# Optimization experiments

Hardware: AMD Instinct MI355X
Metric: run time of the kernel (lower is better)

## Reference

```python
import jax, jax.numpy as jnp
import numpy as np

B, T, C = 2, 2048, 1024
H = 16
D = C // H  # 64
SCALE = 1.0 / np.sqrt(D)


def setup_inputs() -> dict:
    key = jax.random.key(0)
    k1, k2, k3 = jax.random.split(key, 3)
    x = jax.random.normal(k1, (B, T, C), dtype=jnp.float32)
    Wqkv = jax.random.normal(k2, (C, 3 * C), dtype=jnp.float32) * 0.02
    bqkv = jnp.zeros((3 * C,), dtype=jnp.float32)
    Wo = jax.random.normal(k3, (C, C), dtype=jnp.float32) * 0.02
    bo = jnp.zeros((C,), dtype=jnp.float32)
    return {"x": x, "Wqkv": Wqkv, "bqkv": bqkv, "Wo": Wo, "bo": bo}


def reference(x, Wqkv, bqkv, Wo, bo):
    Bsz, Tlen, Cdim = x.shape
    qkv = x @ Wqkv + bqkv                       # [B,T,3C]
    qkv = qkv.reshape(Bsz, Tlen, 3, H, D)
    qkv = jnp.transpose(qkv, (2, 0, 3, 1, 4))   # [3,B,H,T,D]
    q, k, v = qkv[0], qkv[1], qkv[2]
    att = jnp.einsum("bhqd,bhkd->bhqk", q, k) * SCALE
    # NOTE: faithful to source: mask keeps positions where k >= q
    i = jnp.arange(Tlen)
    mask = i[None, :] >= i[:, None]             # [T,T], entry [q,k]: k >= q
    att = jnp.where(mask[None, None], att, -jnp.inf)
    att = jax.nn.softmax(att, axis=-1)
    # dropout p=0.0 (inference) -> identity
    y = jnp.einsum("bhqk,bhkd->bhqd", att, v)   # [B,H,T,D]
    y = jnp.transpose(y, (0, 2, 1, 3)).reshape(Bsz, Tlen, Cdim)
    y = y @ Wo + bo
    return y
```

## Files before the change

### kernel.cpp

```cpp
#include <hip/hip_runtime.h>
#include <hip/hip_bf16.h>
#include <cstdint>
#include <cstddef>

typedef __bf16 bf16_t;
typedef __bf16 bf16x8 __attribute__((ext_vector_type(8)));
typedef __bf16 bf16x4 __attribute__((ext_vector_type(4)));
typedef short short4v __attribute__((ext_vector_type(4)));
typedef float f32x4 __attribute__((ext_vector_type(4)));

#define NB 2
#define NT 2048
#define NC 1024
#define NH 16
#define ND 64
#define NM (NB * NT)
#define N3 (3 * NC)
#define QSCALE_LOG2E 0.18033688011112042f

#define GLOAD_LDS16(gptr, lptr)                                                          \
  __builtin_amdgcn_global_load_lds((const __attribute__((address_space(1))) void*)(gptr), \
                                   (__attribute__((address_space(3))) void*)(lptr), 16, 0, 0)

__global__ __launch_bounds__(256) void prep_k(const float* __restrict__ x,
                                              const float* __restrict__ Wqkv,
                                              const float* __restrict__ Wo,
                                              bf16_t* __restrict__ xbf,
                                              bf16_t* __restrict__ wqkvT,
                                              bf16_t* __restrict__ woT) {
  __shared__ float tile[32][33];
  const int bx = blockIdx.x;
  if (bx < 4096) {
    const int i = (bx * 256 + threadIdx.x) * 4;
    const float4 v = *(const float4*)(x + i);
    bf16x4 o;
    o[0] = (bf16_t)v.x; o[1] = (bf16_t)v.y; o[2] = (bf16_t)v.z; o[3] = (bf16_t)v.w;
    *(bf16x4*)(xbf + i) = o;
    return;
  }
  const int t = bx - 4096;
  const int cxi = t & 127;
  const int tr = (t >> 7) * 32;
  const float* in;
  bf16_t* out;
  int Ccols, tc;
  if (cxi < 96) { in = Wqkv; out = wqkvT; Ccols = 3072; tc = cxi * 32; }
  else          { in = Wo;   out = woT;   Ccols = 1024; tc = (cxi - 96) * 32; }
  const int lx = threadIdx.x & 31;
  const int ly = threadIdx.x >> 5;
#pragma unroll
  for (int i = 0; i < 32; i += 8)
    tile[ly + i][lx] = in[(size_t)(tr + ly + i) * Ccols + tc + lx];
  __syncthreads();
#pragma unroll
  for (int i = 0; i < 32; i += 8)
    out[(size_t)(tc + ly + i) * 1024 + tr + lx] = (bf16_t)tile[lx][ly + i];
}

template <int K>
__device__ __forceinline__ void gemm_mainloop(const bf16_t* __restrict__ A,
                                              const bf16_t* __restrict__ Bt,
                                              int m0, int n0, f32x4 acc[4][4],
                                              bf16_t* lds) {
  bf16_t* As = lds;
  bf16_t* Bs = lds + 4096;
  const int tid = threadIdx.x;
  const int lane = tid & 63;
  const int w = tid >> 6;
  const int wm = (w & 1) * 64;
  const int wn = (w >> 1) * 64;
  const int quad = lane >> 4;
  const int l16 = lane & 15;

  for (int k0 = 0; k0 < K; k0 += 32) {
#pragma unroll
    for (int i = 0; i < 2; ++i) {
      const int gb = w * 128 + i * 64;
      const int g = gb + lane;
      GLOAD_LDS16(A + (size_t)(m0 + (g >> 2)) * K + k0 + (g & 3) * 8, As + gb * 8);
      GLOAD_LDS16(Bt + (size_t)(n0 + (g >> 2)) * K + k0 + (g & 3) * 8, Bs + gb * 8);
    }
    __syncthreads();
    bf16x8 af[4], bfr[4];
#pragma unroll
    for (int i = 0; i < 4; ++i)
      af[i] = *(const bf16x8*)(As + (wm + i * 16 + l16) * 32 + quad * 8);
#pragma unroll
    for (int j = 0; j < 4; ++j)
      bfr[j] = *(const bf16x8*)(Bs + (wn + j * 16 + l16) * 32 + quad * 8);
#pragma unroll
    for (int i = 0; i < 4; ++i)
#pragma unroll
      for (int j = 0; j < 4; ++j)
        acc[i][j] = __builtin_amdgcn_mfma_f32_16x16x32_bf16(af[i], bfr[j], acc[i][j], 0, 0, 0);
    __syncthreads();
  }
}

__global__ __launch_bounds__(256) void qkv_gemm_k(const bf16_t* __restrict__ A,
                                                  const bf16_t* __restrict__ Bt,
                                                  const float* __restrict__ bias,
                                                  bf16_t* __restrict__ qb,
                                                  bf16_t* __restrict__ kb,
                                                  bf16_t* __restrict__ vt2) {
  __shared__ __align__(16) bf16_t lds[8192];
  const int xcd = blockIdx.x & 7;
  const int i2 = blockIdx.x >> 3;
  const int m0 = (i2 & 31) * 128;
  const int n0 = (xcd * 3 + (i2 >> 5)) * 128;
  f32x4 acc[4][4] = {};
  gemm_mainloop<NC>(A, Bt, m0, n0, acc, lds);

  const int lane = threadIdx.x & 63;
  const int w = threadIdx.x >> 6;
  const int wm = (w & 1) * 64, wn = (w >> 1) * 64;
  const int quad = lane >> 4, l16 = lane & 15;
#pragma unroll
  for (int i = 0; i < 4; ++i)
#pragma unroll
    for (int j = 0; j < 4; ++j) {
      const int n = n0 + wn + j * 16 + l16;
      const float bn = bias[n];
      const int which = n >> 10;
      const int rem = n & 1023;
      const int h = rem >> 6, d = rem & 63;
      const int mb = m0 + wm + i * 16 + quad * 4;
      const int b = mb >> 11, t4 = mb & 2047;
      const size_t bh = (size_t)b * NH + h;
      if (which == 2) {
        const int c = t4 >> 6, g = (t4 >> 2) & 15;
        bf16x4 val;
#pragma unroll
        for (int r = 0; r < 4; ++r) val[r] = (bf16_t)(acc[i][j][r] + bn);
        *(bf16x4*)(vt2 + ((bh * 32 + c) * 1024 + (size_t)g * 64 + d) * 4) = val;
      } else {
        bf16_t* dst = (which == 0) ? qb : kb;
        const float sc = (which == 0) ? QSCALE_LOG2E : 1.0f;
#pragma unroll
        for (int r = 0; r < 4; ++r)
          dst[(bh * NT + t4 + r) * ND + d] = (bf16_t)((acc[i][j][r] + bn) * sc);
      }
    }
}

__global__ __launch_bounds__(256, 4) void attn_k(const bf16_t* __restrict__ q,
                                                 const bf16_t* __restrict__ k,
                                                 const bf16_t* __restrict__ vt2,
                                                 bf16_t* __restrict__ y ) {
  const int bh = blockIdx.x & 31;
  const int u = (blockIdx.x >> 5) & 7;
  const int r4 = blockIdx.x >> 8;
  const int T = r4 * 8 + ((r4 & 1) ? (7 - u) : u);
  const int b = bh >> 4, h = bh & 15;

  const bf16_t* qp = q + (size_t)bh * NT * ND;
  const bf16_t* kp = k + (size_t)bh * NT * ND;
  const bf16_t* vp = vt2 + (size_t)bh * 32 * 4096;

  __shared__ __align__(16) bf16_t kbuf0[4096], kbuf1[4096];
  __shared__ __align__(16) bf16_t vbuf0[4096], vbuf1[4096];

  const int lane = threadIdx.x & 63;
  const int w = threadIdx.x >> 6;
  const int quad = lane >> 4, l16 = lane & 15;
  const int qv = T * 64 + w * 16 + l16;

  const bf16x8 qf0 = *(const bf16x8*)(qp + (size_t)qv * ND + quad * 8);
  const bf16x8 qf1 = *(const bf16x8*)(qp + (size_t)qv * ND + 32 + quad * 8);

  const short4v ones = {0x3F80, 0x3F80, 0x3F80, 0x3F80};

  f32x4 zs = {0.f, 0.f, 0.f, 0.f};
  f32x4 o[4];
#pragma unroll
  for (int dj = 0; dj < 4; ++dj) o[dj] = (f32x4){0.f, 0.f, 0.f, 0.f};

  auto stage = [&](int c, bf16_t* kb_, bf16_t* vb_) {
    const bf16_t* kc = kp + (size_t)c * 4096;
    const bf16_t* vc = vp + (size_t)c * 4096;
#pragma unroll
    for (int i = 0; i < 2; ++i) {
      const int gb = w * 128 + i * 64;
      const int s = gb + lane;
      const int row = s >> 3;
      const int cs = (s & 7) ^ (row & 7);
      GLOAD_LDS16(kc + (size_t)row * 64 + cs * 8, kb_ + gb * 8);
      GLOAD_LDS16(vc + (size_t)s * 8, vb_ + gb * 8);
    }
  };

  auto step = [&](const bf16_t* kt, const bf16_t* vt, int c) {
    const int t0 = c * 64;
    f32x4 sv[4];
#pragma unroll
    for (int kj = 0; kj < 4; ++kj) {
      const int kr = kj * 16 + l16;
      const int sw = kr & 7;
      const bf16x8 a0 = *(const bf16x8*)(kt + ((size_t)kr * 8 + (quad ^ sw)) * 8);
      const bf16x8 a1 = *(const bf16x8*)(kt + ((size_t)kr * 8 + ((4 + quad) ^ sw)) * 8);
      f32x4 z = {0.f, 0.f, 0.f, 0.f};
      z = __builtin_amdgcn_mfma_f32_16x16x32_bf16(a0, qf0, z, 0, 0, 0);
      z = __builtin_amdgcn_mfma_f32_16x16x32_bf16(a1, qf1, z, 0, 0, 0);
      sv[kj] = z;
    }
    if (c == T) {
#pragma unroll
      for (int kj = 0; kj < 4; ++kj)
#pragma unroll
        for (int r = 0; r < 4; ++r)
          if (t0 + kj * 16 + quad * 4 + r < qv) sv[kj][r] = -INFINITY;
    }
    short4v pf[4];
#pragma unroll
    for (int kj = 0; kj < 4; ++kj) {
      bf16x4 pb;
#pragma unroll
      for (int r = 0; r < 4; ++r) pb[r] = (bf16_t)__builtin_amdgcn_exp2f(sv[kj][r]);
      pf[kj] = __builtin_bit_cast(short4v, pb);
    }
#pragma unroll
    for (int kj = 0; kj < 4; ++kj)
      zs = __builtin_amdgcn_mfma_f32_16x16x16bf16_1k(ones, pf[kj], zs, 0, 0, 0);
#pragma unroll
    for (int dj = 0; dj < 4; ++dj) {
#pragma unroll
      for (int kj = 0; kj < 4; ++kj) {
        const bf16x4 a =
            *(const bf16x4*)(vt + ((size_t)(kj * 4 + quad) * 64 + dj * 16 + l16) * 4);
        o[dj] = __builtin_amdgcn_mfma_f32_16x16x16bf16_1k(
            __builtin_bit_cast(short4v, a), pf[kj], o[dj], 0, 0, 0);
      }
    }
  };

  stage(T, kbuf0, vbuf0);
  int c = T;
  while (true) {
    __syncthreads();
    if (c + 1 < 32) stage(c + 1, kbuf1, vbuf1);
    step(kbuf0, vbuf0, c);
    if (++c >= 32) break;
    __syncthreads();
    if (c + 1 < 32) stage(c + 1, kbuf0, vbuf0);
    step(kbuf1, vbuf1, c);
    if (++c >= 32) break;
  }

  const float inv = 1.0f / zs[0];
  const size_t base = ((size_t)b * NT + qv) * NC + h * 64;
#pragma unroll
  for (int dj = 0; dj < 4; ++dj) {
    bf16x4 va;
#pragma unroll
    for (int r = 0; r < 4; ++r) va[r] = (bf16_t)(o[dj][r] * inv);
    *(bf16x4*)(y + base + dj * 16 + quad * 4) = va;
  }
}

__global__ __launch_bounds__(256) void out_gemm_k(const bf16_t* __restrict__ A,
                                                  const bf16_t* __restrict__ Bt,
                                                  const float* __restrict__ bias,
                                                  float* __restrict__ out) {
  __shared__ __align__(16) bf16_t lds[8192];
  const int n0 = (blockIdx.x & 7) * 128;
  const int m0 = (blockIdx.x >> 3) * 128;
  f32x4 acc[4][4] = {};
  gemm_mainloop<NC>(A, Bt, m0, n0, acc, lds);

  const int lane = threadIdx.x & 63;
  const int w = threadIdx.x >> 6;
  const int wm = (w & 1) * 64, wn = (w >> 1) * 64;
  const int quad = lane >> 4, l16 = lane & 15;
#pragma unroll
  for (int i = 0; i < 4; ++i)
#pragma unroll
    for (int j = 0; j < 4; ++j) {
      const int n = n0 + wn + j * 16 + l16;
      const float bn = bias[n];
#pragma unroll
      for (int r = 0; r < 4; ++r) {
        const int m = m0 + wm + i * 16 + quad * 4 + r;
        out[(size_t)m * NC + n] = acc[i][j][r] + bn;
      }
    }
}

extern "C" void kernel_launch(void* const* d_in, const int* in_sizes, int n_in,
                              void* d_out, int out_size, void* d_ws, size_t ws_size,
                              hipStream_t stream) {
  const float* x = (const float*)d_in[0];
  const float* Wqkv = (const float*)d_in[1];
  const float* bqkv = (const float*)d_in[2];
  const float* Wo = (const float*)d_in[3];
  const float* bo = (const float*)d_in[4];
  float* out = (float*)d_out;

  char* p = (char*)d_ws;
  bf16_t* xbf = (bf16_t*)p;   p += (size_t)NM * NC * sizeof(bf16_t);
  bf16_t* wqkvT = (bf16_t*)p; p += (size_t)N3 * NC * sizeof(bf16_t);
  bf16_t* woT = (bf16_t*)p;   p += (size_t)NC * NC * sizeof(bf16_t);
  bf16_t* qb = (bf16_t*)p;    p += (size_t)NB * NH * NT * ND * sizeof(bf16_t);
  bf16_t* kb = (bf16_t*)p;    p += (size_t)NB * NH * NT * ND * sizeof(bf16_t);
  bf16_t* vt2 = (bf16_t*)p;   p += (size_t)NB * NH * NT * ND * sizeof(bf16_t);
  bf16_t* yb = (bf16_t*)p;    p += (size_t)NM * NC * sizeof(bf16_t);

  hipLaunchKernelGGL(prep_k, dim3(8192), dim3(256), 0, stream,
                     x, Wqkv, Wo, xbf, wqkvT, woT);
  hipLaunchKernelGGL(qkv_gemm_k, dim3(768), dim3(256), 0, stream,
                     xbf, wqkvT, bqkv, qb, kb, vt2);
  hipLaunchKernelGGL(attn_k, dim3(1024), dim3(256), 0, stream, qb, kb, vt2, yb);
  hipLaunchKernelGGL(out_gemm_k, dim3(256), dim3(256), 0, stream,
                     yb, woT, bo, out);
}
```

Measured before the change: 168.6 us.

## Widen QKV GEMM K-step with XOR-swizzled LDS and halve out-GEMM M-tile

The shared GEMM mainloop is inlined into each kernel and specialized. The QKV GEMM now stages 64-wide K slices with an XOR swizzle on the 16-byte chunks, which halves the number of barriers per K loop and avoids LDS bank conflicts on fragment reads. The output GEMM uses 64-row M tiles, doubling the grid to 512 blocks so more CUs are busy on MI355X. The cost is more LDS per QKV block, which may lower occupancy, and less B-tile reuse in the output GEMM.

```diff
diff --git a/kernel.cpp b/kernel.cpp
--- a/kernel.cpp
+++ b/kernel.cpp
@@ -57,64 +57,57 @@
     out[(size_t)(tc + ly + i) * 1024 + tr + lx] = (bf16_t)tile[lx][ly + i];
 }
 
-template <int K>
-__device__ __forceinline__ void gemm_mainloop(const bf16_t* __restrict__ A,
-                                              const bf16_t* __restrict__ Bt,
-                                              int m0, int n0, f32x4 acc[4][4],
-                                              bf16_t* lds) {
-  bf16_t* As = lds;
-  bf16_t* Bs = lds + 4096;
-  const int tid = threadIdx.x;
-  const int lane = tid & 63;
-  const int w = tid >> 6;
-  const int wm = (w & 1) * 64;
-  const int wn = (w >> 1) * 64;
-  const int quad = lane >> 4;
-  const int l16 = lane & 15;
-
-  for (int k0 = 0; k0 < K; k0 += 32) {
-#pragma unroll
-    for (int i = 0; i < 2; ++i) {
-      const int gb = w * 128 + i * 64;
-      const int g = gb + lane;
-      GLOAD_LDS16(A + (size_t)(m0 + (g >> 2)) * K + k0 + (g & 3) * 8, As + gb * 8);
-      GLOAD_LDS16(Bt + (size_t)(n0 + (g >> 2)) * K + k0 + (g & 3) * 8, Bs + gb * 8);
-    }
-    __syncthreads();
-    bf16x8 af[4], bfr[4];
-#pragma unroll
-    for (int i = 0; i < 4; ++i)
-      af[i] = *(const bf16x8*)(As + (wm + i * 16 + l16) * 32 + quad * 8);
-#pragma unroll
-    for (int j = 0; j < 4; ++j)
-      bfr[j] = *(const bf16x8*)(Bs + (wn + j * 16 + l16) * 32 + quad * 8);
-#pragma unroll
-    for (int i = 0; i < 4; ++i)
-#pragma unroll
-      for (int j = 0; j < 4; ++j)
-        acc[i][j] = __builtin_amdgcn_mfma_f32_16x16x32_bf16(af[i], bfr[j], acc[i][j], 0, 0, 0);
-    __syncthreads();
-  }
-}
-
 __global__ __launch_bounds__(256) void qkv_gemm_k(const bf16_t* __restrict__ A,
                                                   const bf16_t* __restrict__ Bt,
                                                   const float* __restrict__ bias,
                                                   bf16_t* __restrict__ qb,
                                                   bf16_t* __restrict__ kb,
                                                   bf16_t* __restrict__ vt2) {
-  __shared__ __align__(16) bf16_t lds[8192];
+  __shared__ __align__(16) bf16_t lds[16384];
+  bf16_t* As = lds;
+  bf16_t* Bs = lds + 8192;
   const int xcd = blockIdx.x & 7;
   const int i2 = blockIdx.x >> 3;
   const int m0 = (i2 & 31) * 128;
   const int n0 = (xcd * 3 + (i2 >> 5)) * 128;
-  f32x4 acc[4][4] = {};
-  gemm_mainloop<NC>(A, Bt, m0, n0, acc, lds);
 
   const int lane = threadIdx.x & 63;
   const int w = threadIdx.x >> 6;
   const int wm = (w & 1) * 64, wn = (w >> 1) * 64;
   const int quad = lane >> 4, l16 = lane & 15;
+  const int sw = l16 & 7;
+
+  f32x4 acc[4][4] = {};
+
+  for (int k0 = 0; k0 < NC; k0 += 64) {
+#pragma unroll
+    for (int i = 0; i < 4; ++i) {
+      const int gb = w * 256 + i * 64;
+      const int g = gb + lane;
+      const int row = g >> 3;
+      const int cs = (g & 7) ^ (row & 7);
+      GLOAD_LDS16(A + (size_t)(m0 + row) * NC + k0 + cs * 8, As + gb * 8);
+      GLOAD_LDS16(Bt + (size_t)(n0 + row) * NC + k0 + cs * 8, Bs + gb * 8);
+    }
+    __syncthreads();
+#pragma unroll
+    for (int h = 0; h < 2; ++h) {
+      bf16x8 af[4], bfr[4];
+#pragma unroll
+      for (int i = 0; i < 4; ++i)
+        af[i] = *(const bf16x8*)(As + ((wm + i * 16 + l16) * 8 + ((h * 4 + quad) ^ sw)) * 8);
+#pragma unroll
+      for (int j = 0; j < 4; ++j)
+        bfr[j] = *(const bf16x8*)(Bs + ((wn + j * 16 + l16) * 8 + ((h * 4 + quad) ^ sw)) * 8);
+#pragma unroll
+      for (int i = 0; i < 4; ++i)
+#pragma unroll
+        for (int j = 0; j < 4; ++j)
+          acc[i][j] = __builtin_amdgcn_mfma_f32_16x16x32_bf16(af[i], bfr[j], acc[i][j], 0, 0, 0);
+    }
+    __syncthreads();
+  }
+
 #pragma unroll
   for (int i = 0; i < 4; ++i)
 #pragma unroll
@@ -261,18 +254,48 @@
                                                   const bf16_t* __restrict__ Bt,
                                                   const float* __restrict__ bias,
                                                   float* __restrict__ out) {
-  __shared__ __align__(16) bf16_t lds[8192];
+  __shared__ __align__(16) bf16_t lds[6144];
+  bf16_t* As = lds;
+  bf16_t* Bs = lds + 2048;
   const int n0 = (blockIdx.x & 7) * 128;
-  const int m0 = (blockIdx.x >> 3) * 128;
-  f32x4 acc[4][4] = {};
-  gemm_mainloop<NC>(A, Bt, m0, n0, acc, lds);
+  const int m0 = (blockIdx.x >> 3) * 64;
 
   const int lane = threadIdx.x & 63;
   const int w = threadIdx.x >> 6;
-  const int wm = (w & 1) * 64, wn = (w >> 1) * 64;
+  const int wm = (w & 1) * 32, wn = (w >> 1) * 64;
   const int quad = lane >> 4, l16 = lane & 15;
-#pragma unroll
-  for (int i = 0; i < 4; ++i)
+
+  f32x4 acc[2][4] = {};
+
+  for (int k0 = 0; k0 < NC; k0 += 32) {
+    {
+      const int g = w * 64 + lane;
+      GLOAD_LDS16(A + (size_t)(m0 + (g >> 2)) * NC + k0 + (g & 3) * 8, As + w * 64 * 8);
+    }
+#pragma unroll
+    for (int i = 0; i < 2; ++i) {
+      const int gb = w * 128 + i * 64;
+      const int g = gb + lane;
+      GLOAD_LDS16(Bt + (size_t)(n0 + (g >> 2)) * NC + k0 + (g & 3) * 8, Bs + gb * 8);
+    }
+    __syncthreads();
+    bf16x8 af[2], bfr[4];
+#pragma unroll
+    for (int i = 0; i < 2; ++i)
+      af[i] = *(const bf16x8*)(As + ((wm + i * 16 + l16) * 4 + quad) * 8);
+#pragma unroll
+    for (int j = 0; j < 4; ++j)
+      bfr[j] = *(const bf16x8*)(Bs + ((wn + j * 16 + l16) * 4 + quad) * 8);
+#pragma unroll
+    for (int i = 0; i < 2; ++i)
+#pragma unroll
+      for (int j = 0; j < 4; ++j)
+        acc[i][j] = __builtin_amdgcn_mfma_f32_16x16x32_bf16(af[i], bfr[j], acc[i][j], 0, 0, 0);
+    __syncthreads();
+  }
+
+#pragma unroll
+  for (int i = 0; i < 2; ++i)
 #pragma unroll
     for (int j = 0; j < 4; ++j) {
       const int n = n0 + wn + j * 16 + l16;
@@ -309,6 +332,6 @@
   hipLaunchKernelGGL(qkv_gemm_k, dim3(768), dim3(256), 0, stream,
                      xbf, wqkvT, bqkv, qb, kb, vt2);
   hipLaunchKernelGGL(attn_k, dim3(1024), dim3(256), 0, stream, qb, kb, vt2, yb);
-  hipLaunchKernelGGL(out_gemm_k, dim3(256), dim3(256), 0, stream,
+  hipLaunchKernelGGL(out_gemm_k, dim3(512), dim3(256), 0, stream,
                      yb, woT, bo, out);
 }
```

After: 177.8 us. 1.05x slower.
